# Performance work log

Hardware: AMD Instinct MI355X
Metric: run time of the kernel (lower is better)

## Reference

```python
import jax, jax.numpy as jnp
import numpy as np

SCALE_FACTOR = 8.0  # sqrt(head_dim=64)

def setup_inputs() -> dict:
    key = jax.random.key(0)
    kq, kk, kv = jax.random.split(key, 3)
    BH, S, D = 64, 2048, 64  # batch*heads, seq_len, head_dim
    q = jax.random.normal(kq, (BH, S, D), dtype=jnp.float32)
    k = jax.random.normal(kk, (BH, S, D), dtype=jnp.float32)
    v = jax.random.normal(kv, (BH, S, D), dtype=jnp.float32)
    return {"q": q, "k": k, "v": v}

def reference(q, k, v):
    # qk = q @ k^T, scaled, softmax over keys, (dropout p=0 == identity), @ v
    scores = jnp.einsum("bqd,bkd->bqk", q, k) / SCALE_FACTOR  # [BH, S, S]
    attn = jax.nn.softmax(scores, axis=-1)
    out = jnp.einsum("bqk,bkd->bqd", attn, v)  # [BH, S, D]
    return out
```

## Files before the change

### kernel.cpp

```cpp
#include <hip/hip_runtime.h>
#include <hip/hip_bf16.h>


typedef __attribute__((ext_vector_type(8))) short short8;
typedef __attribute__((ext_vector_type(4))) short short4v;
typedef __attribute__((ext_vector_type(4))) float float4v;

#define S_LEN 2048
#define D_DIM 64
#define BH_N  64
#define LOG2E 1.4426950408889634f
#define CLF   (0.125f * LOG2E)

__device__ __forceinline__ unsigned int fpack2_fast(float a, float b) {
    unsigned int ua = __builtin_bit_cast(unsigned int, a) + 0x8000u;
    unsigned int ub = __builtin_bit_cast(unsigned int, b) + 0x8000u;
    return __builtin_amdgcn_perm(ub, ua, 0x07060302);
}
__device__ __forceinline__ void load16_lds(const unsigned short* g, unsigned short* l) {
    __builtin_amdgcn_global_load_lds(
        (const __attribute__((address_space(1))) unsigned int*)g,
        (__attribute__((address_space(3))) unsigned int*)l,
        16, 0, 0);
}

__global__ void __launch_bounds__(256) prep(const float* __restrict__ k,
                                            const float* __restrict__ v,
                                            unsigned short* __restrict__ kbf,
                                            unsigned short* __restrict__ vt) {
    __shared__ unsigned short T[64 * 66];
    const int b = blockIdx.x;
    const int t = threadIdx.x;
    if (b < 4096) {
        const size_t i = ((size_t)b * 256 + t) * 8;
        const float4 a0 = *(const float4*)(k + i);
        const float4 a1 = *(const float4*)(k + i + 4);
        uint4 o;
        o.x = fpack2_fast(a0.x, a0.y); o.y = fpack2_fast(a0.z, a0.w);
        o.z = fpack2_fast(a1.x, a1.y); o.w = fpack2_fast(a1.z, a1.w);
        *(uint4*)(kbf + i) = o;
        return;
    }
    const int idx = b - 4096;
    const int kt = idx & 31, bh = idx >> 5;
    const float* Vg = v + ((size_t)bh * S_LEN + kt * 64) * D_DIM;
    #pragma unroll
    for (int it = 0; it < 4; ++it) {
        const int row = it * 16 + (t >> 4);
        const int col = (t & 15) * 4;
        const float4 f = *(const float4*)(Vg + row * 64 + col);
        unsigned int* p = (unsigned int*)&T[row * 66 + col];
        p[0] = fpack2_fast(f.x, f.y);
        p[1] = fpack2_fast(f.z, f.w);
    }
    __syncthreads();
    const int d  = t >> 2;
    const int kg = t & 3;
    unsigned int w[8];
    #pragma unroll
    for (int j = 0; j < 8; ++j) {
        const unsigned int lo = T[(kg * 16 + 2 * j)     * 66 + d];
        const unsigned int hi = T[(kg * 16 + 2 * j + 1) * 66 + d];
        w[j] = __builtin_amdgcn_perm(hi, lo, 0x05040100);
    }
    unsigned short* out = vt + ((size_t)bh * 64 + d) * S_LEN + kt * 64 + kg * 16;
    uint4 o0; o0.x = w[0]; o0.y = w[1]; o0.z = w[2]; o0.w = w[3];
    uint4 o1; o1.x = w[4]; o1.y = w[5]; o1.z = w[6]; o1.w = w[7];
    *(uint4*)(out)     = o0;
    *(uint4*)(out + 8) = o1;
}

__global__ void __launch_bounds__(256) attn_fwd4(
        const float* __restrict__ q, const unsigned short* __restrict__ kbf,
        const unsigned short* __restrict__ vt, float* __restrict__ out) {
    __shared__ __align__(16) unsigned short Klds[64 * 64];
    __shared__ __align__(16) unsigned short Vlds[64 * 64];

    const int tid  = threadIdx.x;
    const int lane = tid & 63;
    const int wave = tid >> 6;
    const int l16  = lane & 15;
    const int quad = lane >> 4;
    const int rsw  = l16 & 7;

    const int bh    = blockIdx.y;
    const int qbase = blockIdx.x * 128;

    const unsigned short* Kb = kbf + (size_t)bh * S_LEN * D_DIM;
    const unsigned short* Vb = vt  + (size_t)bh * D_DIM * S_LEN;

    short8 qf[2][2];
    #pragma unroll
    for (int s = 0; s < 2; ++s) {
        const int qg = qbase + s * 64 + wave * 16 + l16;
        const float* Qr = q + ((size_t)bh * S_LEN + qg) * D_DIM;
        #pragma unroll
        for (int h = 0; h < 2; ++h) {
            const float4 a = *(const float4*)(Qr + h * 32 + quad * 8);
            const float4 b = *(const float4*)(Qr + h * 32 + quad * 8 + 4);
            uint4 w;
            w.x = fpack2_fast(a.x * CLF, a.y * CLF);
            w.y = fpack2_fast(a.z * CLF, a.w * CLF);
            w.z = fpack2_fast(b.x * CLF, b.y * CLF);
            w.w = fpack2_fast(b.z * CLF, b.w * CLF);
            qf[s][h] = __builtin_bit_cast(short8, w);
        }
    }

    const int srow0  = wave * 16 + (lane >> 3);
    const int schunk = (lane & 7) ^ (lane >> 3);
    unsigned short* kdst0 = &Klds[wave * 1024 + lane * 8];
    unsigned short* vdst0 = &Vlds[wave * 1024 + lane * 8];

    float4v acc[2][4];
    #pragma unroll
    for (int s = 0; s < 2; ++s)
        #pragma unroll
        for (int dt = 0; dt < 4; ++dt) acc[s][dt] = (float4v){0.f, 0.f, 0.f, 0.f};
    float l_acc[2] = {0.f, 0.f};

    for (int kt = 0; kt < S_LEN / 64; ++kt) {
        __syncthreads();
        #pragma unroll
        for (int ss = 0; ss < 2; ++ss) {
            const int row = srow0 + ss * 8;
            load16_lds(Kb + ((size_t)(kt * 64 + row)) * 64 + schunk * 8,
                       kdst0 + ss * 512);
            load16_lds(Vb + (size_t)row * S_LEN + kt * 64 + schunk * 8,
                       vdst0 + ss * 512);
        }
        __syncthreads();

        float4v st[2][4];
        #pragma unroll
        for (int ks = 0; ks < 4; ++ks) {
            const unsigned short* kr = &Klds[(ks * 16 + l16) * 64];
            const int p0 = ((quad ^ rsw) * 8);
            const short8 kf0 = *(const short8*)(kr + p0);
            const short8 kf1 = *(const short8*)(kr + (p0 ^ 32));
            #pragma unroll
            for (int s = 0; s < 2; ++s) {
                float4v z = (float4v){0.f, 0.f, 0.f, 0.f};
                z = __builtin_amdgcn_mfma_f32_16x16x32_bf16(kf0, qf[s][0], z, 0, 0, 0);
                z = __builtin_amdgcn_mfma_f32_16x16x32_bf16(kf1, qf[s][1], z, 0, 0, 0);
                st[s][ks] = z;
            }
        }

        short4v pf[2][4];
        #pragma unroll
        for (int s = 0; s < 2; ++s) {
            #pragma unroll
            for (int ks = 0; ks < 4; ++ks) {
                const float p0 = __builtin_amdgcn_exp2f(st[s][ks][0]);
                const float p1 = __builtin_amdgcn_exp2f(st[s][ks][1]);
                const float p2 = __builtin_amdgcn_exp2f(st[s][ks][2]);
                const float p3 = __builtin_amdgcn_exp2f(st[s][ks][3]);
                l_acc[s] += (p0 + p1) + (p2 + p3);
                uint2 u; u.x = fpack2_fast(p0, p1); u.y = fpack2_fast(p2, p3);
                pf[s][ks] = __builtin_bit_cast(short4v, u);
            }
        }

        #pragma unroll
        for (int dt = 0; dt < 4; ++dt) {
            const unsigned short* vrow = &Vlds[(dt * 16 + l16) * 64 + (quad & 1) * 4];
            #pragma unroll
            for (int ks = 0; ks < 4; ++ks) {
                const int pos16 = (ks * 2 + (quad >> 1)) ^ rsw;
                const short4v vf = *(const short4v*)(vrow + pos16 * 8);
                #pragma unroll
                for (int s = 0; s < 2; ++s)
                    acc[s][dt] = __builtin_amdgcn_mfma_f32_16x16x16bf16_1k(vf, pf[s][ks], acc[s][dt], 0, 0, 0);
            }
        }
    }

    #pragma unroll
    for (int s = 0; s < 2; ++s) {
        float l = l_acc[s];
        l += __shfl_xor(l, 16, 64);
        l += __shfl_xor(l, 32, 64);
        const float inv = 1.0f / l;
        const int qg = qbase + s * 64 + wave * 16 + l16;
        float* Or = out + ((size_t)bh * S_LEN + qg) * D_DIM;
        #pragma unroll
        for (int dt = 0; dt < 4; ++dt) {
            float4 o;
            o.x = acc[s][dt][0] * inv; o.y = acc[s][dt][1] * inv;
            o.z = acc[s][dt][2] * inv; o.w = acc[s][dt][3] * inv;
            *(float4*)(Or + dt * 16 + quad * 4) = o;
        }
    }
}

#define KSTRIDE 72
__device__ __forceinline__ unsigned short bf16_bits(float f) {
    __hip_bfloat16 h = __float2bfloat16(f);
    unsigned short u;
    __builtin_memcpy(&u, &h, sizeof(u));
    return u;
}
__global__ void __launch_bounds__(256) attn_fwd(
        const float* __restrict__ q, const float* __restrict__ k,
        const float* __restrict__ v, float* __restrict__ out) {
    __shared__ __align__(16) unsigned short Klds[64 * KSTRIDE];
    __shared__ __align__(16) unsigned short Vlds[64 * KSTRIDE];
    const int tid  = threadIdx.x;
    const int lane = tid & 63;
    const int wave = tid >> 6;
    const int l16  = lane & 15;
    const int quad = lane >> 4;
    const int bh    = blockIdx.y;
    const int qg    = blockIdx.x * 64 + wave * 16 + l16;
    const float* Qr = q + ((size_t)bh * S_LEN + qg) * D_DIM;
    const float* Kb = k + (size_t)bh * S_LEN * D_DIM;
    const float* Vb = v + (size_t)bh * S_LEN * D_DIM;
    short8 qf[2];
    #pragma unroll
    for (int h = 0; h < 2; ++h) {
        const float4 a = *(const float4*)(Qr + h * 32 + quad * 8);
        const float4 b = *(const float4*)(Qr + h * 32 + quad * 8 + 4);
        uint4 w;
        w.x = fpack2_fast(a.x * CLF, a.y * CLF);
        w.y = fpack2_fast(a.z * CLF, a.w * CLF);
        w.z = fpack2_fast(b.x * CLF, b.y * CLF);
        w.w = fpack2_fast(b.z * CLF, b.w * CLF);
        qf[h] = __builtin_bit_cast(short8, w);
    }
    float4v acc[4];
    #pragma unroll
    for (int dt = 0; dt < 4; ++dt) acc[dt] = (float4v){0.f, 0.f, 0.f, 0.f};
    float l_acc = 0.f;
    for (int kt = 0; kt < S_LEN / 64; ++kt) {
        __syncthreads();
        {
            const float* Kg = Kb + (size_t)kt * 64 * D_DIM;
            #pragma unroll
            for (int i = 0; i < 4; ++i) {
                const int idx = tid + i * 256;
                const int row = idx >> 4;
                const int col = (idx & 15) << 2;
                const float4 f = *(const float4*)(Kg + row * 64 + col);
                uint2 w; w.x = fpack2_fast(f.x, f.y); w.y = fpack2_fast(f.z, f.w);
                *(uint2*)(&Klds[row * KSTRIDE + col]) = w;
            }
        }
        {
            const float* Vg = Vb + (size_t)kt * 64 * D_DIM;
            #pragma unroll
            for (int it = 0; it < 2; ++it) {
                const int rp   = (tid & 15) + (it << 4);
                const int cg   = tid >> 4;
                const int row0 = rp * 2;
                const int col  = cg * 4;
                const float4 a = *(const float4*)(Vg + row0 * 64 + col);
                const float4 b = *(const float4*)(Vg + (row0 + 1) * 64 + col);
                *(unsigned int*)(&Vlds[(col + 0) * KSTRIDE + row0]) = fpack2_fast(a.x, b.x);
                *(unsigned int*)(&Vlds[(col + 1) * KSTRIDE + row0]) = fpack2_fast(a.y, b.y);
                *(unsigned int*)(&Vlds[(col + 2) * KSTRIDE + row0]) = fpack2_fast(a.z, b.z);
                *(unsigned int*)(&Vlds[(col + 3) * KSTRIDE + row0]) = fpack2_fast(a.w, b.w);
            }
        }
        __syncthreads();
        float4v st[4];
        #pragma unroll
        for (int ks = 0; ks < 4; ++ks) {
            const unsigned short* kr = &Klds[(ks * 16 + l16) * KSTRIDE + quad * 8];
            const short8 kf0 = *(const short8*)(kr);
            const short8 kf1 = *(const short8*)(kr + 32);
            float4v z = (float4v){0.f, 0.f, 0.f, 0.f};
            z = __builtin_amdgcn_mfma_f32_16x16x32_bf16(kf0, qf[0], z, 0, 0, 0);
            z = __builtin_amdgcn_mfma_f32_16x16x32_bf16(kf1, qf[1], z, 0, 0, 0);
            st[ks] = z;
        }
        short4v pf[4];
        #pragma unroll
        for (int ks = 0; ks < 4; ++ks) {
            const float p0 = __builtin_amdgcn_exp2f(st[ks][0]);
            const float p1 = __builtin_amdgcn_exp2f(st[ks][1]);
            const float p2 = __builtin_amdgcn_exp2f(st[ks][2]);
            const float p3 = __builtin_amdgcn_exp2f(st[ks][3]);
            l_acc += (p0 + p1) + (p2 + p3);
            uint2 u; u.x = fpack2_fast(p0, p1); u.y = fpack2_fast(p2, p3);
            pf[ks] = __builtin_bit_cast(short4v, u);
        }
        #pragma unroll
        for (int dt = 0; dt < 4; ++dt) {
            const unsigned short* vr = &Vlds[(dt * 16 + l16) * KSTRIDE + quad * 4];
            #pragma unroll
            for (int ks = 0; ks < 4; ++ks) {
                const short4v vf = *(const short4v*)(vr + ks * 16);
                acc[dt] = __builtin_amdgcn_mfma_f32_16x16x16bf16_1k(vf, pf[ks], acc[dt], 0, 0, 0);
            }
        }
    }
    float l = l_acc;
    l += __shfl_xor(l, 16, 64);
    l += __shfl_xor(l, 32, 64);
    const float inv = 1.0f / l;
    float* Or = out + ((size_t)bh * S_LEN + qg) * D_DIM;
    #pragma unroll
    for (int dt = 0; dt < 4; ++dt) {
        float4 o;
        o.x = acc[dt][0] * inv; o.y = acc[dt][1] * inv;
        o.z = acc[dt][2] * inv; o.w = acc[dt][3] * inv;
        *(float4*)(Or + dt * 16 + quad * 4) = o;
    }
}

extern "C" void kernel_launch(void* const* d_in, const int* in_sizes, int n_in,
                              void* d_out, int out_size, void* d_ws, size_t ws_size,
                              hipStream_t stream) {
    const float* q = (const float*)d_in[0];
    const float* k = (const float*)d_in[1];
    const float* v = (const float*)d_in[2];
    float* out = (float*)d_out;
    const size_t need = (size_t)2 * BH_N * S_LEN * D_DIM * sizeof(unsigned short);
    if (ws_size >= need) {
        unsigned short* kbf = (unsigned short*)d_ws;
        unsigned short* vtp = kbf + (size_t)BH_N * S_LEN * D_DIM;
        prep<<<dim3(4096 + BH_N * (S_LEN / 64)), 256, 0, stream>>>(k, v, kbf, vtp);
        attn_fwd4<<<dim3(S_LEN / 128, BH_N), 256, 0, stream>>>(q, kbf, vtp, out);
    } else {
        attn_fwd<<<dim3(S_LEN / 64, BH_N), 256, 0, stream>>>(q, k, v, out);
    }
}
```

Baseline: 238.6 us.

## Double-buffer K/V LDS tiles, interleave prep blocks, truncate P to bf16

The attention kernel now uses two LDS buffers for K and V and issues the next tile's global-to-LDS loads before computing on the current tile. This halves the barriers per tile and overlaps load latency with MFMA work. The prep kernel interleaves K-conversion blocks (now two chunks per block) with V-transpose blocks in half as many launches. The P probabilities are packed to bf16 by truncation instead of rounding, which saves ALU work but adds a small bias. Doubled LDS use may limit occupancy, and the launch bound now asks for 4 blocks per CU.

```diff
diff --git a/kernel.cpp b/kernel.cpp
--- a/kernel.cpp
+++ b/kernel.cpp
@@ -16,6 +16,11 @@
     unsigned int ua = __builtin_bit_cast(unsigned int, a) + 0x8000u;
     unsigned int ub = __builtin_bit_cast(unsigned int, b) + 0x8000u;
     return __builtin_amdgcn_perm(ub, ua, 0x07060302);
+}
+__device__ __forceinline__ unsigned int fpack2_trunc(float a, float b) {
+    return __builtin_amdgcn_perm(__builtin_bit_cast(unsigned int, b),
+                                 __builtin_bit_cast(unsigned int, a),
+                                 0x07060302);
 }
 __device__ __forceinline__ void load16_lds(const unsigned short* g, unsigned short* l) {
     __builtin_amdgcn_global_load_lds(
@@ -31,17 +36,21 @@
     __shared__ unsigned short T[64 * 66];
     const int b = blockIdx.x;
     const int t = threadIdx.x;
-    if (b < 4096) {
-        const size_t i = ((size_t)b * 256 + t) * 8;
-        const float4 a0 = *(const float4*)(k + i);
-        const float4 a1 = *(const float4*)(k + i + 4);
-        uint4 o;
-        o.x = fpack2_fast(a0.x, a0.y); o.y = fpack2_fast(a0.z, a0.w);
-        o.z = fpack2_fast(a1.x, a1.y); o.w = fpack2_fast(a1.z, a1.w);
-        *(uint4*)(kbf + i) = o;
+    if (b & 1) {
+        const int kb = b >> 1;
+        const size_t i = ((size_t)kb * 256 + t) * 16;
+        #pragma unroll
+        for (int j = 0; j < 2; ++j) {
+            const float4 a0 = *(const float4*)(k + i + j * 8);
+            const float4 a1 = *(const float4*)(k + i + j * 8 + 4);
+            uint4 o;
+            o.x = fpack2_fast(a0.x, a0.y); o.y = fpack2_fast(a0.z, a0.w);
+            o.z = fpack2_fast(a1.x, a1.y); o.w = fpack2_fast(a1.z, a1.w);
+            *(uint4*)(kbf + i + j * 8) = o;
+        }
         return;
     }
-    const int idx = b - 4096;
+    const int idx = b >> 1;
     const int kt = idx & 31, bh = idx >> 5;
     const float* Vg = v + ((size_t)bh * S_LEN + kt * 64) * D_DIM;
     #pragma unroll
@@ -70,11 +79,11 @@
     *(uint4*)(out + 8) = o1;
 }
 
-__global__ void __launch_bounds__(256) attn_fwd4(
+__global__ void __launch_bounds__(256, 4) attn_fwd5(
         const float* __restrict__ q, const unsigned short* __restrict__ kbf,
         const unsigned short* __restrict__ vt, float* __restrict__ out) {
-    __shared__ __align__(16) unsigned short Klds[64 * 64];
-    __shared__ __align__(16) unsigned short Vlds[64 * 64];
+    __shared__ __align__(16) unsigned short Klds[2][64 * 64];
+    __shared__ __align__(16) unsigned short Vlds[2][64 * 64];
 
     const int tid  = threadIdx.x;
     const int lane = tid & 63;
@@ -109,8 +118,7 @@
 
     const int srow0  = wave * 16 + (lane >> 3);
     const int schunk = (lane & 7) ^ (lane >> 3);
-    unsigned short* kdst0 = &Klds[wave * 1024 + lane * 8];
-    unsigned short* vdst0 = &Vlds[wave * 1024 + lane * 8];
+    const int dsoff  = wave * 1024 + lane * 8;
 
     float4v acc[2][4];
     #pragma unroll
@@ -119,22 +127,22 @@
         for (int dt = 0; dt < 4; ++dt) acc[s][dt] = (float4v){0.f, 0.f, 0.f, 0.f};
     float l_acc[2] = {0.f, 0.f};
 
-    for (int kt = 0; kt < S_LEN / 64; ++kt) {
-        __syncthreads();
+    auto stage = [&](int kt, int buf) {
         #pragma unroll
         for (int ss = 0; ss < 2; ++ss) {
             const int row = srow0 + ss * 8;
             load16_lds(Kb + ((size_t)(kt * 64 + row)) * 64 + schunk * 8,
-                       kdst0 + ss * 512);
+                       &Klds[buf][dsoff + ss * 512]);
             load16_lds(Vb + (size_t)row * S_LEN + kt * 64 + schunk * 8,
-                       vdst0 + ss * 512);
-        }
-        __syncthreads();
-
+                       &Vlds[buf][dsoff + ss * 512]);
+        }
+    };
+
+    auto tile = [&](int buf) {
         float4v st[2][4];
         #pragma unroll
         for (int ks = 0; ks < 4; ++ks) {
-            const unsigned short* kr = &Klds[(ks * 16 + l16) * 64];
+            const unsigned short* kr = &Klds[buf][(ks * 16 + l16) * 64];
             const int p0 = ((quad ^ rsw) * 8);
             const short8 kf0 = *(const short8*)(kr + p0);
             const short8 kf1 = *(const short8*)(kr + (p0 ^ 32));
@@ -146,7 +154,6 @@
                 st[s][ks] = z;
             }
         }
-
         short4v pf[2][4];
         #pragma unroll
         for (int s = 0; s < 2; ++s) {
@@ -157,14 +164,13 @@
                 const float p2 = __builtin_amdgcn_exp2f(st[s][ks][2]);
                 const float p3 = __builtin_amdgcn_exp2f(st[s][ks][3]);
                 l_acc[s] += (p0 + p1) + (p2 + p3);
-                uint2 u; u.x = fpack2_fast(p0, p1); u.y = fpack2_fast(p2, p3);
+                uint2 u; u.x = fpack2_trunc(p0, p1); u.y = fpack2_trunc(p2, p3);
                 pf[s][ks] = __builtin_bit_cast(short4v, u);
             }
         }
-
         #pragma unroll
         for (int dt = 0; dt < 4; ++dt) {
-            const unsigned short* vrow = &Vlds[(dt * 16 + l16) * 64 + (quad & 1) * 4];
+            const unsigned short* vrow = &Vlds[buf][(dt * 16 + l16) * 64 + (quad & 1) * 4];
             #pragma unroll
             for (int ks = 0; ks < 4; ++ks) {
                 const int pos16 = (ks * 2 + (quad >> 1)) ^ rsw;
@@ -174,6 +180,17 @@
                     acc[s][dt] = __builtin_amdgcn_mfma_f32_16x16x16bf16_1k(vf, pf[s][ks], acc[s][dt], 0, 0, 0);
             }
         }
+    };
+
+    stage(0, 0);
+    #pragma unroll 1
+    for (int kt = 0; kt < S_LEN / 64; kt += 2) {
+        __syncthreads();
+        stage(kt + 1, 1);
+        tile(0);
+        __syncthreads();
+        if (kt + 2 < S_LEN / 64) stage(kt + 2, 0);
+        tile(1);
     }
 
     #pragma unroll
@@ -195,12 +212,6 @@
 }
 
 #define KSTRIDE 72
-__device__ __forceinline__ unsigned short bf16_bits(float f) {
-    __hip_bfloat16 h = __float2bfloat16(f);
-    unsigned short u;
-    __builtin_memcpy(&u, &h, sizeof(u));
-    return u;
-}
 __global__ void __launch_bounds__(256) attn_fwd(
         const float* __restrict__ q, const float* __restrict__ k,
         const float* __restrict__ v, float* __restrict__ out) {
@@ -282,7 +293,7 @@
             const float p2 = __builtin_amdgcn_exp2f(st[ks][2]);
             const float p3 = __builtin_amdgcn_exp2f(st[ks][3]);
             l_acc += (p0 + p1) + (p2 + p3);
-            uint2 u; u.x = fpack2_fast(p0, p1); u.y = fpack2_fast(p2, p3);
+            uint2 u; u.x = fpack2_trunc(p0, p1); u.y = fpack2_trunc(p2, p3);
             pf[ks] = __builtin_bit_cast(short4v, u);
         }
         #pragma unroll
@@ -320,8 +331,8 @@
     if (ws_size >= need) {
         unsigned short* kbf = (unsigned short*)d_ws;
         unsigned short* vtp = kbf + (size_t)BH_N * S_LEN * D_DIM;
-        prep<<<dim3(4096 + BH_N * (S_LEN / 64)), 256, 0, stream>>>(k, v, kbf, vtp);
-        attn_fwd4<<<dim3(S_LEN / 128, BH_N), 256, 0, stream>>>(q, kbf, vtp, out);
+        prep<<<dim3(4096), 256, 0, stream>>>(k, v, kbf, vtp);
+        attn_fwd5<<<dim3(S_LEN / 128, BH_N), 256, 0, stream>>>(q, kbf, vtp, out);
     } else {
         attn_fwd<<<dim3(S_LEN / 64, BH_N), 256, 0, stream>>>(q, k, v, out);
     }
```

Result: faster. 217.6 us (-8.8%).
